# Kernel tuning notes

Hardware: AMD Instinct MI355X
Metric: run time of the kernel (lower is better)

## Reference

```python
import jax, jax.numpy as jnp
import numpy as np

D = 1024
H = 16
HD = D // H


def setup_inputs() -> dict:
    key = jax.random.key(0)
    ks = jax.random.split(key, 9)
    s = 1.0 / np.sqrt(D)
    x = jax.random.normal(ks[0], (2, 2048, D), dtype=jnp.float32)
    Wq = jax.random.uniform(ks[1], (D, D), jnp.float32, -s, s)
    bq = jax.random.uniform(ks[2], (D,), jnp.float32, -s, s)
    Wk = jax.random.uniform(ks[3], (D, D), jnp.float32, -s, s)
    bk = jax.random.uniform(ks[4], (D,), jnp.float32, -s, s)
    Wv = jax.random.uniform(ks[5], (D, D), jnp.float32, -s, s)
    bv = jax.random.uniform(ks[6], (D,), jnp.float32, -s, s)
    Wo = jax.random.uniform(ks[7], (D, D), jnp.float32, -s, s)
    bo = jax.random.uniform(ks[8], (D,), jnp.float32, -s, s)
    return {"x": x, "Wq": Wq, "bq": bq, "Wk": Wk, "bk": bk,
            "Wv": Wv, "bv": bv, "Wo": Wo, "bo": bo}


def reference(x, Wq, bq, Wk, bk, Wv, bv, Wo, bo):
    B, S, _ = x.shape
    # project and split heads -> [B, H, S, HD]
    def split(t):
        return t.reshape(B, S, H, HD).transpose(0, 2, 1, 3)
    q = split(x @ Wq + bq)
    k = split(x @ Wk + bk)
    v = split(x @ Wv + bv)
    scores = jnp.einsum('bhqd,bhkd->bhqk', q, k) / np.sqrt(HD).astype(np.float32)
    attn = jax.nn.softmax(scores, axis=-1)
    ctx = jnp.einsum('bhqk,bhkd->bhqd', attn, v)  # [B,H,S,HD]
    ctx = ctx.transpose(0, 2, 1, 3).reshape(B, S, D)
    return ctx @ Wo + bo
```

## Files before the change

kernel.cpp:

```cpp
#include <hip/hip_runtime.h>
#include <hip/hip_bf16.h>
#include <math.h>

#define BB 2
#define SS 2048
#define DD 1024
#define HH 16
#define HD 64
#define MM (BB * SS)
#define NT (SS / 64)

typedef __bf16 bf16;
typedef __attribute__((ext_vector_type(8))) __bf16 bf16x8;
typedef __attribute__((ext_vector_type(4))) __bf16 bf16x4;
typedef __attribute__((ext_vector_type(4))) float f32x4;
typedef __attribute__((ext_vector_type(4))) unsigned u32x4;

#define QSCL 0.18033688011112042f

__device__ __forceinline__ void glds16(const bf16* g, bf16* l) {
    __builtin_amdgcn_global_load_lds(
        (const __attribute__((address_space(1))) void*)g,
        (__attribute__((address_space(3))) void*)l, 16, 0, 0);
}

__device__ __forceinline__ unsigned cvtpk_bf16(float a, float b) {
    unsigned r;
    asm("v_cvt_pk_bf16_f32 %0, %1, %2" : "=v"(r) : "v"(a), "v"(b));
    return r;
}

__global__ __launch_bounds__(256) void cvt_prep(
    const float* __restrict__ x, bf16* __restrict__ xb,
    const float* __restrict__ W0, const float* __restrict__ W1,
    const float* __restrict__ W2, const float* __restrict__ W3,
    bf16* __restrict__ Wt) {
    __shared__ float T[64][65];
    const int bid = blockIdx.x;
    if (bid < 4096) {
        int i = (bid * 256 + threadIdx.x) * 4;
        float4 v = *(const float4*)(x + i);
        bf16x4 o;
        o[0] = (bf16)v.x; o[1] = (bf16)v.y; o[2] = (bf16)v.z; o[3] = (bf16)v.w;
        *(bf16x4*)(xb + i) = o;
        return;
    }
    const int b = bid - 4096;
    const int z = b >> 8;
    const float* W = (z == 0) ? W0 : (z == 1) ? W1 : (z == 2) ? W2 : W3;
    bf16* dst = Wt + (size_t)z * DD * DD;
    int k0 = ((b >> 4) & 15) * 64, n0 = (b & 15) * 64;
    int tr = threadIdx.x >> 4, tc = (threadIdx.x & 15) * 4;
#pragma unroll
    for (int u = 0; u < 4; u++) {
        int r = tr + u * 16;
        float4 v = *(const float4*)&W[(size_t)(k0 + r) * DD + n0 + tc];
        T[tc + 0][r] = v.x; T[tc + 1][r] = v.y;
        T[tc + 2][r] = v.z; T[tc + 3][r] = v.w;
    }
    __syncthreads();
#pragma unroll
    for (int u = 0; u < 4; u++) {
        int r = tr + u * 16;
        bf16x4 o;
        o[0] = (bf16)T[r][tc + 0]; o[1] = (bf16)T[r][tc + 1];
        o[2] = (bf16)T[r][tc + 2]; o[3] = (bf16)T[r][tc + 3];
        *(bf16x4*)&dst[(size_t)(n0 + r) * DD + k0 + tc] = o;
    }
}

__global__ __launch_bounds__(256) void mfma_gemm(
    const bf16* __restrict__ A, const bf16* __restrict__ Wt0,
    const float* __restrict__ b0, const float* __restrict__ b1,
    const float* __restrict__ b2,
    bf16* __restrict__ o0, bf16* __restrict__ o1, bf16* __restrict__ o2) {
    const int z = blockIdx.z;
    const bf16* Wt = Wt0 + (size_t)z * DD * DD;
    const float* bias = (z == 0) ? b0 : (z == 1) ? b1 : b2;
    const float scl = (z == 0) ? QSCL : 1.0f;

    __shared__ __align__(16) bf16 As[128 * 64];
    __shared__ __align__(16) bf16 Bs[128 * 64];

    const int tid = threadIdx.x;
    const int lane = tid & 63;
    const int w = tid >> 6;
    const int l15 = lane & 15, quad = lane >> 4;
    const int m0 = blockIdx.y * 128;
    const int n0 = blockIdx.x * 128;
    const int mw = (w & 1) * 64;
    const int nw = (w >> 1) * 64;

    f32x4 acc[4][4];
#pragma unroll
    for (int i = 0; i < 4; i++)
#pragma unroll
        for (int j = 0; j < 4; j++) acc[i][j] = (f32x4){0.f, 0.f, 0.f, 0.f};

    for (int kt = 0; kt < DD; kt += 64) {
        __syncthreads();
#pragma unroll
        for (int u = 0; u < 4; u++) {
            int j = tid + u * 256;
            int row = j >> 3, cp = j & 7;
            int c = cp ^ (row & 7);
            glds16(A  + (size_t)(m0 + row) * DD + kt + c * 8, &As[j * 8]);
            glds16(Wt + (size_t)(n0 + row) * DD + kt + c * 8, &Bs[j * 8]);
        }
        __syncthreads();

#pragma unroll
        for (int kh = 0; kh < 2; kh++) {
            bf16x8 af[4], bf[4];
#pragma unroll
            for (int i = 0; i < 4; i++) {
                int ra = mw + i * 16 + l15;
                int ja = ra * 8 + ((kh * 4 + quad) ^ (ra & 7));
                af[i] = *(const bf16x8*)&As[ja * 8];
                int rb = nw + i * 16 + l15;
                int jb = rb * 8 + ((kh * 4 + quad) ^ (rb & 7));
                bf[i] = *(const bf16x8*)&Bs[jb * 8];
            }
#pragma unroll
            for (int i = 0; i < 4; i++)
#pragma unroll
                for (int j = 0; j < 4; j++)
                    acc[i][j] = __builtin_amdgcn_mfma_f32_16x16x32_bf16(
                        af[i], bf[j], acc[i][j], 0, 0, 0);
        }
    }

    float bcol[4];
#pragma unroll
    for (int j = 0; j < 4; j++) bcol[j] = bias[n0 + nw + j * 16 + l15];

    if (z == 2) {
        const int mbase = m0 + mw;
        const int bb = (mbase >= SS) ? 1 : 0;
        const int sw = mbase & (SS - 1);
#pragma unroll
        for (int i = 0; i < 4; i++) {
            int scol = sw + (i >> 1) * 32 + quad * 8 + (i & 1) * 4;
#pragma unroll
            for (int j = 0; j < 4; j++) {
                int dg = n0 + nw + j * 16 + l15;
                int h = dg >> 6, d = dg & 63;
                bf16* dst = o2 + ((size_t)(bb * HH + h) * HD + d) * SS + scol;
                bf16x4 ov;
#pragma unroll
                for (int r = 0; r < 4; r++)
                    ov[r] = (bf16)(acc[i][j][r] + bcol[j]);
                *(bf16x4*)dst = ov;
            }
        }
    } else {
        bf16* dstb = (z == 0) ? o0 : o1;
#pragma unroll
        for (int i = 0; i < 4; i++)
#pragma unroll
            for (int j = 0; j < 4; j++)
#pragma unroll
                for (int r = 0; r < 4; r++) {
                    int row = m0 + mw + i * 16 + quad * 4 + r;
                    int col = n0 + nw + j * 16 + l15;
                    dstb[(size_t)row * DD + col] =
                        (bf16)((acc[i][j][r] + bcol[j]) * scl);
                }
    }
}

__global__ __launch_bounds__(256) void mfma_gemm_out(
    const bf16* __restrict__ A, const bf16* __restrict__ Wt,
    const float* __restrict__ bias, float* __restrict__ out) {
    __shared__ __align__(16) bf16 As[64 * 64];
    __shared__ __align__(16) bf16 Bs[128 * 64];

    const int tid = threadIdx.x;
    const int lane = tid & 63;
    const int w = tid >> 6;
    const int l15 = lane & 15, quad = lane >> 4;
    const int m0 = blockIdx.y * 64;
    const int n0 = blockIdx.x * 128;
    const int mw = (w & 1) * 32;
    const int nw = (w >> 1) * 64;

    f32x4 acc[2][4];
#pragma unroll
    for (int i = 0; i < 2; i++)
#pragma unroll
        for (int j = 0; j < 4; j++) acc[i][j] = (f32x4){0.f, 0.f, 0.f, 0.f};

    for (int kt = 0; kt < DD; kt += 64) {
        __syncthreads();
#pragma unroll
        for (int u = 0; u < 2; u++) {
            int j = tid + u * 256;
            int row = j >> 3, c = (j & 7) ^ (row & 7);
            glds16(A + (size_t)(m0 + row) * DD + kt + c * 8, &As[j * 8]);
        }
#pragma unroll
        for (int u = 0; u < 4; u++) {
            int j = tid + u * 256;
            int row = j >> 3, c = (j & 7) ^ (row & 7);
            glds16(Wt + (size_t)(n0 + row) * DD + kt + c * 8, &Bs[j * 8]);
        }
        __syncthreads();

#pragma unroll
        for (int kh = 0; kh < 2; kh++) {
            bf16x8 af[2], bf[4];
#pragma unroll
            for (int i = 0; i < 2; i++) {
                int ra = mw + i * 16 + l15;
                int ja = ra * 8 + ((kh * 4 + quad) ^ (ra & 7));
                af[i] = *(const bf16x8*)&As[ja * 8];
            }
#pragma unroll
            for (int j = 0; j < 4; j++) {
                int rb = nw + j * 16 + l15;
                int jb = rb * 8 + ((kh * 4 + quad) ^ (rb & 7));
                bf[j] = *(const bf16x8*)&Bs[jb * 8];
            }
#pragma unroll
            for (int i = 0; i < 2; i++)
#pragma unroll
                for (int j = 0; j < 4; j++)
                    acc[i][j] = __builtin_amdgcn_mfma_f32_16x16x32_bf16(
                        af[i], bf[j], acc[i][j], 0, 0, 0);
        }
    }

    float bcol[4];
#pragma unroll
    for (int j = 0; j < 4; j++) bcol[j] = bias[n0 + nw + j * 16 + l15];

#pragma unroll
    for (int i = 0; i < 2; i++)
#pragma unroll
        for (int j = 0; j < 4; j++)
#pragma unroll
            for (int r = 0; r < 4; r++) {
                int row = m0 + mw + i * 16 + quad * 4 + r;
                int col = n0 + nw + j * 16 + l15;
                out[(size_t)row * DD + col] = acc[i][j][r] + bcol[j];
            }
}

__global__ __launch_bounds__(256) void mfma_attn(
    const bf16* __restrict__ Qb, const bf16* __restrict__ Kb,
    const bf16* __restrict__ Vtg, bf16* __restrict__ ctxb) {
    __shared__ __align__(16) bf16 Ks[2][64 * 64];
    __shared__ __align__(16) bf16 Vs[2][64 * 64];

    const int tid = threadIdx.x;
    const int lane = tid & 63;
    const int w = tid >> 6;
    const int l15 = lane & 15, quad = lane >> 4;
    const int bh = blockIdx.y;
    const int b = bh >> 4, h = bh & 15;
    const int q0 = blockIdx.x * 64;
    const size_t mb = (size_t)b * SS;
    const int hc = h * HD;
    const bf16* Vt_bh = Vtg + (size_t)bh * HD * SS;

    bf16x8 qf[2];
#pragma unroll
    for (int kh = 0; kh < 2; kh++)
        qf[kh] = *(const bf16x8*)&Qb[(mb + q0 + w * 16 + l15) * DD +
                                     hc + kh * 32 + quad * 8];

    bf16x8 onev;
#pragma unroll
    for (int i = 0; i < 8; i++) onev[i] = (bf16)1.0f;
    const f32x4 zf = (f32x4){0.f, 0.f, 0.f, 0.f};

    int koff[4][2], voff[4][2];
#pragma unroll
    for (int kb = 0; kb < 4; kb++) {
        int rk = kb * 16 + l15;
#pragma unroll
        for (int kh = 0; kh < 2; kh++)
            koff[kb][kh] = (rk * 8 + ((kh * 4 + quad) ^ (rk & 7))) * 8;
    }
#pragma unroll
    for (int nb = 0; nb < 4; nb++) {
        int rv = nb * 16 + l15;
#pragma unroll
        for (int kh = 0; kh < 2; kh++)
            voff[nb][kh] = (rv * 8 + ((kh * 4 + quad) ^ (rv & 7))) * 8;
    }

    const bf16* gK[2]; const bf16* gV[2]; int lo_[2];
#pragma unroll
    for (int u = 0; u < 2; u++) {
        int j = tid + u * 256;
        int row = j >> 3, cp = j & 7;
        int c = cp ^ (row & 7);
        gK[u] = Kb + (mb + row) * DD + hc + c * 8;
        gV[u] = Vt_bh + (size_t)row * SS + c * 8;
        lo_[u] = j * 8;
    }

    f32x4 o[4], lsum;
    lsum = (f32x4){0.f, 0.f, 0.f, 0.f};
#pragma unroll
    for (int nb = 0; nb < 4; nb++) o[nb] = (f32x4){0.f, 0.f, 0.f, 0.f};

#pragma unroll
    for (int u = 0; u < 2; u++) {
        glds16(gK[u], &Ks[0][lo_[u]]);  gK[u] += 64 * DD;
        glds16(gV[u], &Vs[0][lo_[u]]);  gV[u] += 64;
    }
    __syncthreads();

    f32x4 scA[4];
#pragma unroll
    for (int kb = 0; kb < 4; kb++) {
        bf16x8 kf0 = *(const bf16x8*)&Ks[0][koff[kb][0]];
        bf16x8 kf1 = *(const bf16x8*)&Ks[0][koff[kb][1]];
        f32x4 t = __builtin_amdgcn_mfma_f32_16x16x32_bf16(
            kf0, qf[0], zf, 0, 0, 0);
        scA[kb] = __builtin_amdgcn_mfma_f32_16x16x32_bf16(
            kf1, qf[1], t, 0, 0, 0);
    }

    int buf = 0;
    for (int it = 0; it < NT; ++it) {
        const bool more = (it + 1 < NT);
        if (more) {
#pragma unroll
            for (int u = 0; u < 2; u++) {
                glds16(gK[u], &Ks[buf ^ 1][lo_[u]]);  gK[u] += 64 * DD;
                glds16(gV[u], &Vs[buf ^ 1][lo_[u]]);  gV[u] += 64;
            }
        }

        u32x4 pw[2];
#pragma unroll
        for (int kb = 0; kb < 4; kb++) {
            float p0 = exp2f(scA[kb][0]);
            float p1 = exp2f(scA[kb][1]);
            float p2 = exp2f(scA[kb][2]);
            float p3 = exp2f(scA[kb][3]);
            pw[kb >> 1][(kb & 1) * 2 + 0] = cvtpk_bf16(p0, p1);
            pw[kb >> 1][(kb & 1) * 2 + 1] = cvtpk_bf16(p2, p3);
        }
        bf16x8 pfr[2];
        pfr[0] = __builtin_bit_cast(bf16x8, pw[0]);
        pfr[1] = __builtin_bit_cast(bf16x8, pw[1]);

        __syncthreads();

        __builtin_amdgcn_s_setprio(1);
        f32x4 scB[4];
        if (more) {
#pragma unroll
            for (int kb = 0; kb < 4; kb++) {
                bf16x8 kf0 = *(const bf16x8*)&Ks[buf ^ 1][koff[kb][0]];
                bf16x8 kf1 = *(const bf16x8*)&Ks[buf ^ 1][koff[kb][1]];
                f32x4 t = __builtin_amdgcn_mfma_f32_16x16x32_bf16(
                    kf0, qf[0], zf, 0, 0, 0);
                scB[kb] = __builtin_amdgcn_mfma_f32_16x16x32_bf16(
                    kf1, qf[1], t, 0, 0, 0);
            }
        }
#pragma unroll
        for (int kh = 0; kh < 2; kh++) {
            lsum = __builtin_amdgcn_mfma_f32_16x16x32_bf16(
                pfr[kh], onev, lsum, 0, 0, 0);
#pragma unroll
            for (int nb = 0; nb < 4; nb++) {
                bf16x8 vf = *(const bf16x8*)&Vs[buf][voff[nb][kh]];
                o[nb] = __builtin_amdgcn_mfma_f32_16x16x32_bf16(
                    pfr[kh], vf, o[nb], 0, 0, 0);
            }
        }
        __builtin_amdgcn_s_setprio(0);

        __syncthreads();

        if (more) {
#pragma unroll
            for (int kb = 0; kb < 4; kb++) scA[kb] = scB[kb];
        }
        buf ^= 1;
    }

    float li[4];
#pragma unroll
    for (int r = 0; r < 4; r++) li[r] = 1.0f / lsum[r];
#pragma unroll
    for (int nb = 0; nb < 4; nb++)
#pragma unroll
        for (int r = 0; r < 4; r++) {
            int qrow = q0 + w * 16 + quad * 4 + r;
            ctxb[(mb + qrow) * DD + hc + nb * 16 + l15] =
                (bf16)(o[nb][r] * li[r]);
        }
}

extern "C" void kernel_launch(void* const* d_in, const int* in_sizes, int n_in,
                              void* d_out, int out_size, void* d_ws, size_t ws_size,
                              hipStream_t stream) {
    const float* x  = (const float*)d_in[0];
    const float* Wq = (const float*)d_in[1];
    const float* bq = (const float*)d_in[2];
    const float* Wk = (const float*)d_in[3];
    const float* bk = (const float*)d_in[4];
    const float* Wv = (const float*)d_in[5];
    const float* bv = (const float*)d_in[6];
    const float* Wo = (const float*)d_in[7];
    const float* bo = (const float*)d_in[8];
    float* out = (float*)d_out;

    char* base = (char*)d_ws;
    bf16* xb   = (bf16*)(base);
    bf16* Wt   = (bf16*)(base + (8ull  << 20));
    bf16* Qb   = (bf16*)(base + (16ull << 20));
    bf16* Kb   = (bf16*)(base + (24ull << 20));
    bf16* Vt   = (bf16*)(base + (32ull << 20));
    bf16* ctxb = (bf16*)(base + (40ull << 20));

    cvt_prep<<<dim3(4096 + 1024), dim3(256), 0, stream>>>(
        x, xb, Wq, Wk, Wv, Wo, Wt);

    mfma_gemm<<<dim3(DD / 128, MM / 128, 3), dim3(256), 0, stream>>>(
        xb, Wt, bq, bk, bv, Qb, Kb, Vt);

    mfma_attn<<<dim3(SS / 64, BB * HH), dim3(256), 0, stream>>>(Qb, Kb, Vt, ctxb);

    mfma_gemm_out<<<dim3(DD / 128, MM / 64), dim3(256), 0, stream>>>(
        ctxb, Wt + 3ull * DD * DD, bo, out);
}
```

Baseline: 219.4 us.

## Remap block indices for XCD-local L2 reuse and use polynomial exp2

All three compute kernels now launch a 1D grid and remap the linear block id so that blocks dispatched round-robin to the same XCD (lin&7) work on contiguous tiles. This is meant to improve L2 reuse of shared A/B tiles and K/V within each XCD. Separately, the attention softmax replaces exp2f with a degree-4 polynomial plus ldexpf, moving exponentiation from the transcendental unit onto FMA pipes. The polynomial slightly reduces accuracy, and the results are rounded to bf16 anyway.

```diff
diff --git a/kernel.cpp b/kernel.cpp
--- a/kernel.cpp
+++ b/kernel.cpp
@@ -28,6 +28,16 @@
     unsigned r;
     asm("v_cvt_pk_bf16_f32 %0, %1, %2" : "=v"(r) : "v"(a), "v"(b));
     return r;
+}
+
+__device__ __forceinline__ float exp2p(float s) {
+    float n = rintf(s);
+    float f = s - n;
+    float p = fmaf(f, 0.00961812910f, 0.0555041087f);
+    p = fmaf(f, p, 0.240226507f);
+    p = fmaf(f, p, 0.693147180f);
+    p = fmaf(f, p, 1.0f);
+    return ldexpf(p, (int)n);
 }
 
 __global__ __launch_bounds__(256) void cvt_prep(
@@ -74,7 +84,13 @@
     const float* __restrict__ b0, const float* __restrict__ b1,
     const float* __restrict__ b2,
     bf16* __restrict__ o0, bf16* __restrict__ o1, bf16* __restrict__ o2) {
-    const int z = blockIdx.z;
+    const int lin = blockIdx.x;
+    const int nl = (lin & 7) * 96 + (lin >> 3);
+    const int z = nl >> 8;
+    const int rem = nl & 255;
+    const int m0 = (rem >> 3) * 128;
+    const int n0 = (rem & 7) * 128;
+
     const bf16* Wt = Wt0 + (size_t)z * DD * DD;
     const float* bias = (z == 0) ? b0 : (z == 1) ? b1 : b2;
     const float scl = (z == 0) ? QSCL : 1.0f;
@@ -86,8 +102,6 @@
     const int lane = tid & 63;
     const int w = tid >> 6;
     const int l15 = lane & 15, quad = lane >> 4;
-    const int m0 = blockIdx.y * 128;
-    const int n0 = blockIdx.x * 128;
     const int mw = (w & 1) * 64;
     const int nw = (w >> 1) * 64;
 
@@ -172,6 +186,11 @@
 __global__ __launch_bounds__(256) void mfma_gemm_out(
     const bf16* __restrict__ A, const bf16* __restrict__ Wt,
     const float* __restrict__ bias, float* __restrict__ out) {
+    const int lin = blockIdx.x;
+    const int nl = (lin & 7) * 64 + (lin >> 3);
+    const int m0 = (nl >> 3) * 64;
+    const int n0 = (nl & 7) * 128;
+
     __shared__ __align__(16) bf16 As[64 * 64];
     __shared__ __align__(16) bf16 Bs[128 * 64];
 
@@ -179,8 +198,6 @@
     const int lane = tid & 63;
     const int w = tid >> 6;
     const int l15 = lane & 15, quad = lane >> 4;
-    const int m0 = blockIdx.y * 64;
-    const int n0 = blockIdx.x * 128;
     const int mw = (w & 1) * 32;
     const int nw = (w >> 1) * 64;
 
@@ -252,13 +269,16 @@
     __shared__ __align__(16) bf16 Ks[2][64 * 64];
     __shared__ __align__(16) bf16 Vs[2][64 * 64];
 
+    const int lin = blockIdx.x;
+    const int nl = (lin & 7) * 128 + (lin >> 3);
+    const int bh = nl >> 5;
+    const int q0 = (nl & 31) * 64;
+
     const int tid = threadIdx.x;
     const int lane = tid & 63;
     const int w = tid >> 6;
     const int l15 = lane & 15, quad = lane >> 4;
-    const int bh = blockIdx.y;
     const int b = bh >> 4, h = bh & 15;
-    const int q0 = blockIdx.x * 64;
     const size_t mb = (size_t)b * SS;
     const int hc = h * HD;
     const bf16* Vt_bh = Vtg + (size_t)bh * HD * SS;
@@ -338,10 +358,10 @@
         u32x4 pw[2];
 #pragma unroll
         for (int kb = 0; kb < 4; kb++) {
-            float p0 = exp2f(scA[kb][0]);
-            float p1 = exp2f(scA[kb][1]);
-            float p2 = exp2f(scA[kb][2]);
-            float p3 = exp2f(scA[kb][3]);
+            float p0 = exp2p(scA[kb][0]);
+            float p1 = exp2p(scA[kb][1]);
+            float p2 = exp2p(scA[kb][2]);
+            float p3 = exp2p(scA[kb][3]);
             pw[kb >> 1][(kb & 1) * 2 + 0] = cvtpk_bf16(p0, p1);
             pw[kb >> 1][(kb & 1) * 2 + 1] = cvtpk_bf16(p2, p3);
         }
@@ -424,11 +444,11 @@
     cvt_prep<<<dim3(4096 + 1024), dim3(256), 0, stream>>>(
         x, xb, Wq, Wk, Wv, Wo, Wt);
 
-    mfma_gemm<<<dim3(DD / 128, MM / 128, 3), dim3(256), 0, stream>>>(
+    mfma_gemm<<<dim3(768), dim3(256), 0, stream>>>(
         xb, Wt, bq, bk, bv, Qb, Kb, Vt);
 
-    mfma_attn<<<dim3(SS / 64, BB * HH), dim3(256), 0, stream>>>(Qb, Kb, Vt, ctxb);
-
-    mfma_gemm_out<<<dim3(DD / 128, MM / 64), dim3(256), 0, stream>>>(
+    mfma_attn<<<dim3(1024), dim3(256), 0, stream>>>(Qb, Kb, Vt, ctxb);
+
+    mfma_gemm_out<<<dim3(512), dim3(256), 0, stream>>>(
         ctxb, Wt + 3ull * DD * DD, bo, out);
 }
```

Result: faster. 208.4 us (-5.0%).
